# Kernel optimization log

Measured on AMD Instinct MI355X. Metric: run time of the kernel, lower is better.

Reference implementation:

```python
import jax, jax.numpy as jnp
import numpy as np

NQ = 4  # n_qubits
NL = 2  # n_qlayers


def _rx(state, theta, wire):
    # state: (B, 2,...,2) complex; theta: (B,) RX rotation angles
    c = jnp.cos(theta * 0.5)[:, None]
    s = jnp.sin(theta * 0.5)[:, None]
    st = jnp.moveaxis(state, wire + 1, 1)
    sh = st.shape
    st = st.reshape(sh[0], 2, -1)
    a0, a1 = st[:, 0], st[:, 1]
    n0 = c * a0 - 1j * s * a1
    n1 = -1j * s * a0 + c * a1
    st = jnp.stack([n0, n1], axis=1).reshape(sh)
    return jnp.moveaxis(st, 1, wire + 1)


def _cnot(state, ctrl, tgt):
    st = jnp.moveaxis(state, (ctrl + 1, tgt + 1), (1, 2))
    st = jnp.stack([st[:, 0], st[:, 1, ::-1]], axis=1)
    return jnp.moveaxis(st, (1, 2), (ctrl + 1, tgt + 1))


def _vqc(y, W):
    # AngleEmbedding (RX) + BasicEntanglerLayers (RX + CNOT ring), PauliZ expvals.
    # y: (B, NQ) angles; W: (NL, NQ); returns (B, NQ)
    B = y.shape[0]
    state = jnp.zeros((B,) + (2,) * NQ, jnp.complex64)
    state = state.at[(slice(None),) + (0,) * NQ].set(1.0)
    for w in range(NQ):
        state = _rx(state, y[:, w], w)
    for l in range(W.shape[0]):
        for w in range(NQ):
            state = _rx(state, jnp.broadcast_to(W[l, w], (B,)), w)
        for w in range(NQ):
            state = _cnot(state, w, (w + 1) % NQ)
    probs = state.real ** 2 + state.imag ** 2  # (B, 2,2,2,2)
    z = jnp.array([1.0, -1.0], probs.dtype)
    exps = []
    for w in range(NQ):
        sign = z.reshape((1,) + (1,) * w + (2,) + (1,) * (NQ - 1 - w))
        exps.append(jnp.sum(probs * sign, axis=tuple(range(1, NQ + 1))))
    return jnp.stack(exps, axis=1)


def setup_inputs() -> dict:
    key = jax.random.key(0)
    ks = jax.random.split(key, 12)
    B, T, F, H = 1024, 64, 32, 8
    two_pi = 2.0 * np.pi
    return {
        "x": jax.random.normal(ks[0], (B, T, F), jnp.float32),
        "w_in": jax.random.normal(ks[1], (NQ, F + H), jnp.float32) * 0.1,
        "b_in": jnp.zeros((NQ,), jnp.float32),
        "w_out": jax.random.normal(ks[2], (H, NQ), jnp.float32) * 0.1,
        "b_out": jnp.zeros((H,), jnp.float32),
        "wq_f": jax.random.uniform(ks[3], (NL, NQ), jnp.float32, 0.0, two_pi),
        "wq_i": jax.random.uniform(ks[4], (NL, NQ), jnp.float32, 0.0, two_pi),
        "wq_u": jax.random.uniform(ks[5], (NL, NQ), jnp.float32, 0.0, two_pi),
        "wq_o": jax.random.uniform(ks[6], (NL, NQ), jnp.float32, 0.0, two_pi),
        "w_fc": jax.random.normal(ks[7], (1, H), jnp.float32) * 0.1,
        "b_fc": jnp.zeros((1,), jnp.float32),
    }


def reference(x, w_in, b_in, w_out, b_out, wq_f, wq_i, wq_u, wq_o, w_fc, b_fc):
    B, T, F = x.shape
    H = w_out.shape[0]
    h0 = jnp.zeros((B, H), x.dtype)
    c0 = jnp.zeros((B, H), x.dtype)

    def step(carry, x_t):
        h, c = carry
        v = jnp.concatenate([h, x_t], axis=1)           # (B, H+F)
        y = v @ w_in.T + b_in                           # (B, NQ)
        gate = lambda Wq: _vqc(y, Wq) @ w_out.T + b_out  # (B, H)
        f = jax.nn.sigmoid(gate(wq_f))
        i = jax.nn.sigmoid(gate(wq_i))
        g = jnp.tanh(gate(wq_u))
        o = jax.nn.sigmoid(gate(wq_o))
        c = f * c + i * g
        h = o * jnp.tanh(c)
        return (h, c), None

    (h, c), _ = jax.lax.scan(step, (h0, c0), jnp.swapaxes(x, 0, 1))
    return h @ w_fc.T + b_fc  # (B, 1)
```

## Files before the change

kernel.cpp:

```cpp
#include <hip/hip_runtime.h>
#include <math.h>


#define NQ 4
#define NL 2
#define BB 1024
#define TT 64
#define FF 32
#define HH 8

typedef unsigned uv2 __attribute__((ext_vector_type(2)));

#define QUAD_BCAST(x, CTRL) \
    __int_as_float(__builtin_amdgcn_mov_dpp(__float_as_int(x), (CTRL), 0xf, 0xf, true))
#define ROW_ROR(x, N) \
    __int_as_float(__builtin_amdgcn_mov_dpp(__float_as_int(x), 0x120 + (N), 0xf, 0xf, true))
#define SWZ_X16(x) \
    __int_as_float(__builtin_amdgcn_ds_swizzle(__float_as_int(x), 0x401F))

#if __has_builtin(__builtin_amdgcn_permlane16_swap)
__device__ __forceinline__ float permx16(float s, int lane) {
    uv2 r = __builtin_amdgcn_permlane16_swap(__builtin_bit_cast(unsigned, s),
                                             __builtin_bit_cast(unsigned, s),
                                             false, false);
    unsigned pick = (lane & 16) ? r.x : r.y;
    return __builtin_bit_cast(float, pick);
}
#else
__device__ __forceinline__ float permx16(float s, int lane) {
    (void)lane;
    return SWZ_X16(s);
}
#endif

#define XSTRIDE 68

__global__ __launch_bounds__(64, 1)
void qlstm_hb_kernel(const float* __restrict__ x,
                     const float* __restrict__ w_in,
                     const float* __restrict__ b_in,
                     const float* __restrict__ w_out,
                     const float* __restrict__ b_out,
                     const float* __restrict__ wq_f,
                     const float* __restrict__ wq_i,
                     const float* __restrict__ wq_u,
                     const float* __restrict__ wq_o,
                     const float* __restrict__ w_fc,
                     const float* __restrict__ b_fc,
                     float* __restrict__ out) {
    __shared__ __align__(16) float sXW[8 * XSTRIDE];

    const int lane = threadIdx.x;
    const int w    = lane & 3;
    const int j    = (lane >> 2) & 7;
    const int e    = lane >> 5;

    {
        const float b0 = b_in[0], b1 = b_in[1], b2 = b_in[2], b3 = b_in[3];
        #pragma unroll
        for (int r = 0; r < 8; ++r) {
            int slot = lane + 64 * r;
            int ee = slot >> 8;
            int tt = (slot >> 2) & 63;
            int ww = slot & 3;
            const float* xr = x + ((size_t)(blockIdx.x * 2 + ee) * TT + tt) * FF;
            float bb = (ww == 0) ? b0 : (ww == 1) ? b1 : (ww == 2) ? b2 : b3;
            const float* wrow = w_in + ww * 40 + 8;
            float acc0 = bb, acc1 = 0.0f;
            #pragma unroll
            for (int k = 0; k < 8; k += 2) {
                float4 xa = *reinterpret_cast<const float4*>(xr + 4 * k);
                float4 xb = *reinterpret_cast<const float4*>(xr + 4 * k + 4);
                acc0 = fmaf(xa.x, wrow[4*k+0],
                       fmaf(xa.y, wrow[4*k+1],
                       fmaf(xa.z, wrow[4*k+2],
                       fmaf(xa.w, wrow[4*k+3], acc0))));
                acc1 = fmaf(xb.x, wrow[4*k+4],
                       fmaf(xb.y, wrow[4*k+5],
                       fmaf(xb.z, wrow[4*k+6],
                       fmaf(xb.w, wrow[4*k+7], acc1))));
            }
            sXW[(ee * 4 + ww) * XSTRIDE + tt] = acc0 + acc1;
        }
    }
    __syncthreads();

    const float* wq = (w == 0) ? wq_f : (w == 1) ? wq_i : (w == 2) ? wq_u : wq_o;
    const float cph0 = __cosf(wq[0]), sph0 = __sinf(wq[0]);
    const float cph1 = __cosf(wq[1]), sph1 = __sinf(wq[1]);
    const float cph2 = __cosf(wq[2]), sph2 = __sinf(wq[2]);
    const float cph3 = __cosf(wq[3]), sph3 = __sinf(wq[3]);
    const float c0 = __cosf(wq[4]), s0 = __sinf(wq[4]);
    const float c1 = __cosf(wq[5]), s1 = __sinf(wq[5]);
    const float c2 = __cosf(wq[6]), s2 = __sinf(wq[6]);
    const float c3 = __cosf(wq[7]), s3 = __sinf(wq[7]);
    const float wo0 = w_out[j * 4 + 0], wo1 = w_out[j * 4 + 1];
    const float wo2 = w_out[j * 4 + 2], wo3 = w_out[j * 4 + 3];
    const float g0a = wo0 * (c1 * c2 * c3);
    const float g0b = wo0 * (c1 * c2 * s3);
    const float g0c = wo0 * (s1 * s2 * c3);
    const float g0d = wo0 * (s1 * s2 * s3);
    const float g1a = wo1 * (c0 * c1);
    const float g1b = wo1 * (s0 * s1);
    const float g2a = wo2 * (c0 * c1 * c2);
    const float g2b = wo2 * (c0 * s1 * s2);
    const float g3a = wo3 * (c0 * c1 * c2 * c3);
    const float g3b = wo3 * (s0 * s1 * c2 * c3);
    const float g3c = wo3 * (s0 * c1 * s2 * s3);
    const float g3d = wo3 * (c0 * s1 * s2 * s3);
    const float bo  = b_out[j];

    const float wh  = w_in[w * 40 + j];
    const float wfc = w_fc[j];
    const bool  isG  = (w == 2);
    const float inS  = isG ? 2.0f : 1.0f;
    const float outS = isG ? 2.0f : 1.0f;
    const float outB = isG ? -1.0f : 0.0f;

    const float* sxw = sXW + (e * 4 + w) * XSTRIDE;

    float cc = 0.0f, hh = 0.0f;

#define STEP(xwv) do {                                                        \
          \
    float p_ = hh * wh;                                                       \
    float s_ = p_ + ROW_ROR(p_, 4);                                           \
    s_ = s_ + ROW_ROR(s_, 8);                                                 \
    const float y_ = (xwv) + s_ + permx16(s_, lane);                          \
    const float u_ = __cosf(y_), v_ = __sinf(y_);                             \
    const float u0_ = QUAD_BCAST(u_, 0x00), u1_ = QUAD_BCAST(u_, 0x55);       \
    const float u2_ = QUAD_BCAST(u_, 0xAA), u3_ = QUAD_BCAST(u_, 0xFF);       \
    const float v0_ = QUAD_BCAST(v_, 0x00), v1_ = QUAD_BCAST(v_, 0x55);       \
    const float v2_ = QUAD_BCAST(v_, 0xAA), v3_ = QUAD_BCAST(v_, 0xFF);       \
         \
    const float t0_ = fmaf(cph0, u0_, -(sph0 * v0_));                         \
    const float t1_ = fmaf(cph1, u1_, -(sph1 * v1_));                         \
    const float t2_ = fmaf(cph2, u2_, -(sph2 * v2_));                         \
    const float t3_ = fmaf(cph3, u3_, -(sph3 * v3_));                         \
    const float r0_ = fmaf(sph0, u0_, cph0 * v0_);                            \
    const float r1_ = fmaf(sph1, u1_, cph1 * v1_);                            \
    const float r2_ = fmaf(sph2, u2_, cph2 * v2_);                            \
    const float r3_ = fmaf(sph3, u3_, cph3 * v3_);                            \
                                                           \
    const float P_ = t1_ * t3_;                                               \
    const float Q_ = r1_ * r3_;                                               \
    const float S_ = t0_ * t2_;                                               \
    const float T_ = r0_ * r2_;                                               \
    const float U_ = t0_ * r2_;                                               \
    const float V_ = r0_ * t2_;                                               \
                                                  \
    const float mP_ = fmaf(g0a, t0_, fmaf(g0d, r0_, g2a));                    \
    const float mQ_ = fmaf(g0c, t0_, fmaf(g0b, r0_, g2b));                    \
    float a_ = fmaf(mP_, P_, fmaf(mQ_, Q_, bo));                              \
    const float e1_ = fmaf(g1a, S_, g1b * T_);                                \
    a_ = fmaf(e1_, t3_, a_);                                                  \
    a_ = fmaf(g3a, S_, a_);                                                   \
    a_ = fmaf(g3b, T_, a_);                                                   \
    a_ = fmaf(g3c, U_, a_);                                                   \
    a_ = fmaf(g3d, V_, a_);                                                   \
                     \
    const float sg_ = __builtin_amdgcn_rcpf(1.0f + __expf(-inS * a_));        \
    const float act_ = fmaf(sg_, outS, outB);                                 \
    const float fv_ = QUAD_BCAST(act_, 0x00), iv_ = QUAD_BCAST(act_, 0x55);   \
    const float gv_ = QUAD_BCAST(act_, 0xAA), ov_ = QUAD_BCAST(act_, 0xFF);   \
    cc = fmaf(fv_, cc, iv_ * gv_);                                            \
    const float th_ = fmaf(2.0f,                                              \
        __builtin_amdgcn_rcpf(1.0f + __expf(-2.0f * cc)), -1.0f);             \
    hh = ov_ * th_;                                                           \
} while (0)

    float4 xq = *reinterpret_cast<const float4*>(sxw);
    #pragma unroll 1
    for (int g4 = 0; g4 < 16; ++g4) {
        const int nx = (g4 < 15) ? (g4 + 1) * 4 : 60;
        float4 xqn = *reinterpret_cast<const float4*>(sxw + nx);
        STEP(xq.x);
        STEP(xq.y);
        STEP(xq.z);
        STEP(xq.w);
        xq = xqn;
    }
#undef STEP

    float pf = hh * wfc;
    float sf = pf + ROW_ROR(pf, 4);
    sf = sf + ROW_ROR(sf, 8);
    sf = sf + permx16(sf, lane);
    if ((lane & 31) == 0) out[blockIdx.x * 2 + e] = sf + b_fc[0];
}

extern "C" void kernel_launch(void* const* d_in, const int* in_sizes, int n_in,
                              void* d_out, int out_size, void* d_ws, size_t ws_size,
                              hipStream_t stream) {
    const float* x     = (const float*)d_in[0];
    const float* w_in  = (const float*)d_in[1];
    const float* b_in  = (const float*)d_in[2];
    const float* w_out = (const float*)d_in[3];
    const float* b_out = (const float*)d_in[4];
    const float* wq_f  = (const float*)d_in[5];
    const float* wq_i  = (const float*)d_in[6];
    const float* wq_u  = (const float*)d_in[7];
    const float* wq_o  = (const float*)d_in[8];
    const float* w_fc  = (const float*)d_in[9];
    const float* b_fc  = (const float*)d_in[10];
    float* out = (float*)d_out;
    (void)in_sizes; (void)n_in; (void)out_size; (void)d_ws; (void)ws_size;

    qlstm_hb_kernel<<<BB / 2, 64, 0, stream>>>(x, w_in, b_in, w_out, b_out,
                                               wq_f, wq_i, wq_u, wq_o,
                                               w_fc, b_fc, out);
}
```

Before: 88.96 us.

## Interleave two independent batch chains per wavefront to hide recurrence latency

Each 64-lane wavefront now handles four batch rows in two independent recurrence chains (A and B), with their time steps interleaved. The grid is halved to 256 blocks, and the shared-memory precompute of the input projection doubles to cover four rows. The point is to hide the serial latency of each step (DPP shuffles, transcendentals, dependent FMAs) with independent work from the other chain. The cost is fewer blocks than the 256 CUs can host at high occupancy, more register pressure, and twice the per-block prologue work.

Result: slower. 99.33 us (+11.7%).

```diff
diff --git a/kernel.cpp b/kernel.cpp
--- a/kernel.cpp
+++ b/kernel.cpp
@@ -36,19 +36,19 @@
 #define XSTRIDE 68
 
 __global__ __launch_bounds__(64, 1)
-void qlstm_hb_kernel(const float* __restrict__ x,
-                     const float* __restrict__ w_in,
-                     const float* __restrict__ b_in,
-                     const float* __restrict__ w_out,
-                     const float* __restrict__ b_out,
-                     const float* __restrict__ wq_f,
-                     const float* __restrict__ wq_i,
-                     const float* __restrict__ wq_u,
-                     const float* __restrict__ wq_o,
-                     const float* __restrict__ w_fc,
-                     const float* __restrict__ b_fc,
-                     float* __restrict__ out) {
-    __shared__ __align__(16) float sXW[8 * XSTRIDE];
+void qlstm_hb2_kernel(const float* __restrict__ x,
+                      const float* __restrict__ w_in,
+                      const float* __restrict__ b_in,
+                      const float* __restrict__ w_out,
+                      const float* __restrict__ b_out,
+                      const float* __restrict__ wq_f,
+                      const float* __restrict__ wq_i,
+                      const float* __restrict__ wq_u,
+                      const float* __restrict__ wq_o,
+                      const float* __restrict__ w_fc,
+                      const float* __restrict__ b_fc,
+                      float* __restrict__ out) {
+    __shared__ __align__(16) float sXW[16 * XSTRIDE];
 
     const int lane = threadIdx.x;
     const int w    = lane & 3;
@@ -58,12 +58,12 @@
     {
         const float b0 = b_in[0], b1 = b_in[1], b2 = b_in[2], b3 = b_in[3];
         #pragma unroll
-        for (int r = 0; r < 8; ++r) {
+        for (int r = 0; r < 16; ++r) {
             int slot = lane + 64 * r;
             int ee = slot >> 8;
             int tt = (slot >> 2) & 63;
             int ww = slot & 3;
-            const float* xr = x + ((size_t)(blockIdx.x * 2 + ee) * TT + tt) * FF;
+            const float* xr = x + ((size_t)(blockIdx.x * 4 + ee) * TT + tt) * FF;
             float bb = (ww == 0) ? b0 : (ww == 1) ? b1 : (ww == 2) ? b2 : b3;
             const float* wrow = w_in + ww * 40 + 8;
             float acc0 = bb, acc1 = 0.0f;
@@ -117,13 +117,13 @@
     const float outS = isG ? 2.0f : 1.0f;
     const float outB = isG ? -1.0f : 0.0f;
 
-    const float* sxw = sXW + (e * 4 + w) * XSTRIDE;
-
-    float cc = 0.0f, hh = 0.0f;
-
-#define STEP(xwv) do {                                                        \
-          \
-    float p_ = hh * wh;                                                       \
+    const float* pA = sXW + ((e)     * 4 + w) * XSTRIDE;
+    const float* pB = sXW + ((e + 2) * 4 + w) * XSTRIDE;
+
+    float ccA = 0.0f, hhA = 0.0f, ccB = 0.0f, hhB = 0.0f;
+
+#define STEP(xwv, cc, hh) do {                                                \
+    float p_ = (hh) * wh;                                                     \
     float s_ = p_ + ROW_ROR(p_, 4);                                           \
     s_ = s_ + ROW_ROR(s_, 8);                                                 \
     const float y_ = (xwv) + s_ + permx16(s_, lane);                          \
@@ -132,7 +132,6 @@
     const float u2_ = QUAD_BCAST(u_, 0xAA), u3_ = QUAD_BCAST(u_, 0xFF);       \
     const float v0_ = QUAD_BCAST(v_, 0x00), v1_ = QUAD_BCAST(v_, 0x55);       \
     const float v2_ = QUAD_BCAST(v_, 0xAA), v3_ = QUAD_BCAST(v_, 0xFF);       \
-         \
     const float t0_ = fmaf(cph0, u0_, -(sph0 * v0_));                         \
     const float t1_ = fmaf(cph1, u1_, -(sph1 * v1_));                         \
     const float t2_ = fmaf(cph2, u2_, -(sph2 * v2_));                         \
@@ -141,14 +140,12 @@
     const float r1_ = fmaf(sph1, u1_, cph1 * v1_);                            \
     const float r2_ = fmaf(sph2, u2_, cph2 * v2_);                            \
     const float r3_ = fmaf(sph3, u3_, cph3 * v3_);                            \
-                                                           \
     const float P_ = t1_ * t3_;                                               \
     const float Q_ = r1_ * r3_;                                               \
     const float S_ = t0_ * t2_;                                               \
     const float T_ = r0_ * r2_;                                               \
     const float U_ = t0_ * r2_;                                               \
     const float V_ = r0_ * t2_;                                               \
-                                                  \
     const float mP_ = fmaf(g0a, t0_, fmaf(g0d, r0_, g2a));                    \
     const float mQ_ = fmaf(g0c, t0_, fmaf(g0b, r0_, g2b));                    \
     float a_ = fmaf(mP_, P_, fmaf(mQ_, Q_, bo));                              \
@@ -158,35 +155,44 @@
     a_ = fmaf(g3b, T_, a_);                                                   \
     a_ = fmaf(g3c, U_, a_);                                                   \
     a_ = fmaf(g3d, V_, a_);                                                   \
-                     \
     const float sg_ = __builtin_amdgcn_rcpf(1.0f + __expf(-inS * a_));        \
     const float act_ = fmaf(sg_, outS, outB);                                 \
     const float fv_ = QUAD_BCAST(act_, 0x00), iv_ = QUAD_BCAST(act_, 0x55);   \
     const float gv_ = QUAD_BCAST(act_, 0xAA), ov_ = QUAD_BCAST(act_, 0xFF);   \
-    cc = fmaf(fv_, cc, iv_ * gv_);                                            \
+    (cc) = fmaf(fv_, (cc), iv_ * gv_);                                        \
     const float th_ = fmaf(2.0f,                                              \
-        __builtin_amdgcn_rcpf(1.0f + __expf(-2.0f * cc)), -1.0f);             \
-    hh = ov_ * th_;                                                           \
+        __builtin_amdgcn_rcpf(1.0f + __expf(-2.0f * (cc))), -1.0f);           \
+    (hh) = ov_ * th_;                                                         \
 } while (0)
 
-    float4 xq = *reinterpret_cast<const float4*>(sxw);
+    float4 xqA = *reinterpret_cast<const float4*>(pA);
+    float4 xqB = *reinterpret_cast<const float4*>(pB);
     #pragma unroll 1
     for (int g4 = 0; g4 < 16; ++g4) {
         const int nx = (g4 < 15) ? (g4 + 1) * 4 : 60;
-        float4 xqn = *reinterpret_cast<const float4*>(sxw + nx);
-        STEP(xq.x);
-        STEP(xq.y);
-        STEP(xq.z);
-        STEP(xq.w);
-        xq = xqn;
+        float4 xqAn = *reinterpret_cast<const float4*>(pA + nx);
+        float4 xqBn = *reinterpret_cast<const float4*>(pB + nx);
+        STEP(xqA.x, ccA, hhA); STEP(xqB.x, ccB, hhB);
+        STEP(xqA.y, ccA, hhA); STEP(xqB.y, ccB, hhB);
+        STEP(xqA.z, ccA, hhA); STEP(xqB.z, ccB, hhB);
+        STEP(xqA.w, ccA, hhA); STEP(xqB.w, ccB, hhB);
+        xqA = xqAn; xqB = xqBn;
     }
 #undef STEP
 
-    float pf = hh * wfc;
-    float sf = pf + ROW_ROR(pf, 4);
-    sf = sf + ROW_ROR(sf, 8);
-    sf = sf + permx16(sf, lane);
-    if ((lane & 31) == 0) out[blockIdx.x * 2 + e] = sf + b_fc[0];
+    float pfA = hhA * wfc;
+    float sfA = pfA + ROW_ROR(pfA, 4);
+    sfA = sfA + ROW_ROR(sfA, 8);
+    sfA = sfA + permx16(sfA, lane);
+    float pfB = hhB * wfc;
+    float sfB = pfB + ROW_ROR(pfB, 4);
+    sfB = sfB + ROW_ROR(sfB, 8);
+    sfB = sfB + permx16(sfB, lane);
+    if ((lane & 31) == 0) {
+        const int base = blockIdx.x * 4 + e;
+        out[base]     = sfA + b_fc[0];
+        out[base + 2] = sfB + b_fc[0];
+    }
 }
 
 extern "C" void kernel_launch(void* const* d_in, const int* in_sizes, int n_in,
@@ -206,7 +212,7 @@
     float* out = (float*)d_out;
     (void)in_sizes; (void)n_in; (void)out_size; (void)d_ws; (void)ws_size;
 
-    qlstm_hb_kernel<<<BB / 2, 64, 0, stream>>>(x, w_in, b_in, w_out, b_out,
-                                               wq_f, wq_i, wq_u, wq_o,
-                                               w_fc, b_fc, out);
-}
+    qlstm_hb2_kernel<<<BB / 4, 64, 0, stream>>>(x, w_in, b_in, w_out, b_out,
+                                                wq_f, wq_i, wq_u, wq_o,
+                                                w_fc, b_fc, out);
+}
```
